# Performance work log

Measured on AMD Instinct MI355X. Metric: run time of the kernel, lower is better.

Reference implementation:

```python
import jax, jax.numpy as jnp
import numpy as np

LAYERS, BLOCKS = 10, 4
DC, RC, SC, CLASSES, K = 128, 128, 512, 256, 2
OUT_LEN = 2 ** (LAYERS - 1)  # 512
N, L = 4, 8192


def _dilations():
    # replicates the (new_dilation, init_dilation) schedule from __init__
    dils = []
    init_d = 1
    for _ in range(BLOCKS):
        d = 1
        for _ in range(LAYERS):
            dils.append((d, init_d))
            init_d = d
            d *= 2
    return dils


def conv1d(x, w):
    # x: (n, c_in, l), w: (c_out, c_in, k), VALID causal-style conv
    return jax.lax.conv_general_dilated(x, w, (1,), 'VALID',
                                        dimension_numbers=('NCH', 'OIH', 'NCH'))


def dilate(x, dilation, init_dilation):
    # fast-wavenet dilate: fold time phases into the batch dim (all shapes static)
    n, c, l = x.shape
    if dilation == init_dilation:
        return x
    if dilation > init_dilation:
        f = dilation // init_dilation
        new_l = -(-l // f) * f  # ceil to multiple of f
        if new_l != l:
            x = jnp.pad(x, ((0, 0), (0, 0), (new_l - l, 0)))  # zero-pad at start
            l = new_l
        l_new, n_new = l // f, n * f
    else:
        f = init_dilation // dilation
        l_new, n_new = l * f, n // f
    # (n,c,l) -> (c,l,n) -> (c,l_new,n_new) -> (n_new,c,l_new), matches torch view order
    x = jnp.transpose(x, (1, 2, 0)).reshape(c, l_new, n_new)
    return jnp.transpose(x, (2, 0, 1))


def setup_inputs() -> dict:
    key = jax.random.key(0)
    ks = jax.random.split(key, 7)
    NL = LAYERS * BLOCKS
    s = 0.05
    return {
        'input': jax.random.normal(ks[0], (N, 1, L), jnp.float32),
        'start_w': jax.random.normal(ks[1], (RC, 1, 1), jnp.float32) * s,
        'dilated_w': jax.random.normal(ks[2], (NL, 2 * DC, RC, K), jnp.float32) * s,
        'residual_w': jax.random.normal(ks[3], (NL, RC, DC, 1), jnp.float32) * s,
        'skip_w': jax.random.normal(ks[4], (NL, SC, DC, 1), jnp.float32) * s,
        'end_w': jax.random.normal(ks[5], (CLASSES, SC, 1), jnp.float32) * s,
        'end_b': jax.random.normal(ks[6], (CLASSES,), jnp.float32) * s,
    }


def reference(input, start_w, dilated_w, residual_w, skip_w, end_w, end_b):
    x = conv1d(input, start_w)
    skip = None
    for i, (d, init_d) in enumerate(_dilations()):
        residual = dilate(x, d, init_d)            # (n*d, RC, l_d)
        h = conv1d(residual, dilated_w[i])          # (n*d, 2*DC, l_d-1)
        h = jnp.tanh(h[:, :DC, :]) * jax.nn.sigmoid(h[:, DC:, :])
        s = dilate(h, 1, d) if h.shape[2] != 1 else h  # back to batch-major time
        s = conv1d(s, skip_w[i])
        skip = s if skip is None else s + skip[:, :, -s.shape[2]:]
        x = conv1d(h, residual_w[i]) + residual[:, :, K - 1:]
    out = conv1d(jax.nn.relu(skip), end_w) + end_b[None, :, None]
    n, c, _ = out.shape
    out = out[:, :, -OUT_LEN:]
    return jnp.transpose(out, (0, 2, 1)).reshape(n * OUT_LEN, c)
```

## Files before the change

### kernel.cpp

```cpp
#include <hip/hip_runtime.h>
#include <stdint.h>

#define NB 4
#define LSEQ 8192
#define TLOC 4608
#define TBASE 3584
#define NLAYER 40
#define SKIP_T0 4096
#define SKIP_LEN 512
#define NCLS 256

typedef float f32x4 __attribute__((ext_vector_type(4)));
typedef short bf16x8 __attribute__((ext_vector_type(8)));

typedef const __attribute__((address_space(1))) uint32_t GU32;
typedef __attribute__((address_space(3))) uint32_t LU32;

__device__ __forceinline__ void gload16(const void* g, void* l) {
    __builtin_amdgcn_global_load_lds((GU32*)g, (LU32*)l, 16, 0, 0);
}

__device__ __forceinline__ uint16_t f2bf(float x) {
    uint32_t u = __builtin_bit_cast(uint32_t, x);
    uint32_t r = (u + 0x7FFFu + ((u >> 16) & 1u)) >> 16;
    return (uint16_t)r;
}
__device__ __forceinline__ float bf2f(uint16_t h) {
    uint32_t u = ((uint32_t)h) << 16;
    return __builtin_bit_cast(float, u);
}
__device__ __forceinline__ uint2 pack4(const uint16_t a[4]) {
    return make_uint2((uint32_t)a[0] | ((uint32_t)a[1] << 16),
                      (uint32_t)a[2] | ((uint32_t)a[3] << 16));
}

__global__ __launch_bounds__(256) void k_prep_a(const float* __restrict__ Wd,
                                                uint16_t* __restrict__ AgH,
                                                uint16_t* __restrict__ AgL) {
    __shared__ float tile[32][257];
    int bi = blockIdx.x;
    int i = bi >> 3;
    int co0 = (bi & 7) * 32;
    int tid = threadIdx.x;
    #pragma unroll
    for (int e = 0; e < 32; ++e) {
        int idx = e * 256 + tid;
        int co_l = idx >> 8, rem = idx & 255;
        tile[co_l][rem] = Wd[(size_t)(i * 256 + co0 + co_l) * 256 + rem];
    }
    __syncthreads();
    #pragma unroll
    for (int e = 0; e < 32; ++e) {
        int co_l = e;
        int kk = tid;
        int ci = kk & 127, kt = kk >> 7;
        float v = tile[co_l][ci * 2 + kt];
        uint16_t h = f2bf(v);
        uint16_t lo = f2bf(v - bf2f(h));
        int co = co0 + co_l;
        int ch = kk >> 5, kkc = kk & 31;
        size_t o = ((size_t)(i * 8 + ch) * 256 + co) * 32 + (kkc ^ (((co >> 1) & 3) << 3));
        AgH[o] = h;
        AgL[o] = lo;
    }
}

__global__ __launch_bounds__(256) void k_prep_w(const float* __restrict__ Wr, const float* __restrict__ Ws,
                                                uint16_t* __restrict__ WrH, uint16_t* __restrict__ WrL,
                                                uint16_t* __restrict__ WsH, uint16_t* __restrict__ WsL) {
    int idx4 = (blockIdx.x * 256 + threadIdx.x) * 4;
    const int NR = NLAYER * 16384;
    const float* src = (idx4 < NR) ? (Wr + idx4) : (Ws + (idx4 - NR));
    uint16_t* dH = (idx4 < NR) ? (WrH + idx4) : (WsH + (idx4 - NR));
    uint16_t* dL = (idx4 < NR) ? (WrL + idx4) : (WsL + (idx4 - NR));
    float4 v = *(const float4*)src;
    uint16_t h[4], lo[4];
    float vv[4] = {v.x, v.y, v.z, v.w};
    #pragma unroll
    for (int r = 0; r < 4; ++r) {
        h[r] = f2bf(vv[r]);
        lo[r] = f2bf(vv[r] - bf2f(h[r]));
    }
    *(uint2*)dH = pack4(h);
    *(uint2*)dL = pack4(lo);
}

__global__ __launch_bounds__(256) void k_prep_e(const float* __restrict__ Ew,
                                                float* __restrict__ ET) {
    int idx = blockIdx.x * 256 + threadIdx.x;
    int cl = idx & 255;
    int sc = idx >> 8;
    ET[sc * 256 + cl] = Ew[cl * 512 + sc];
}

__global__ __launch_bounds__(256) void k_start(const float* __restrict__ input,
                                               const float* __restrict__ sw,
                                               uint16_t* __restrict__ Xh, uint16_t* __restrict__ Xl) {
    int n = blockIdx.y;
    int inner = blockIdx.x * 256 + threadIdx.x;
    int t = inner >> 7, c = inner & 127;
    float x = sw[c] * input[n * LSEQ + TBASE + t];
    uint16_t h = f2bf(x);
    size_t o = (size_t)(n * TLOC + t) * 128 + c;
    Xh[o] = h;
    Xl[o] = f2bf(x - bf2f(h));
}

__global__ __launch_bounds__(256, 2) void k_layer(
    const uint16_t* __restrict__ XhIn, const uint16_t* __restrict__ XlIn,
    uint16_t* __restrict__ XhOut, uint16_t* __restrict__ XlOut,
    float* __restrict__ skipbuf,
    const uint16_t* __restrict__ AgH, const uint16_t* __restrict__ AgL,
    const uint16_t* __restrict__ WrH, const uint16_t* __restrict__ WrL,
    const uint16_t* __restrict__ WsH, const uint16_t* __restrict__ WsL,
    int d)
{
    __shared__ uint16_t As[2][16384];
    __shared__ uint16_t Bs[2][2048];

    const int tid = threadIdx.x;
    const int w  = tid >> 6;
    const int l  = tid & 63;
    const int g  = l >> 4;
    const int lq = l & 15;
    const int tb = 143 - blockIdx.x;
    const int t0 = tb * 32;
    const int nb = blockIdx.y;

    f32x4 acc[2][2][2];
    #pragma unroll
    for (int pm = 0; pm < 2; ++pm)
        #pragma unroll
        for (int mi = 0; mi < 2; ++mi)
            #pragma unroll
            for (int ni = 0; ni < 2; ++ni)
                acc[pm][mi][ni] = (f32x4){0.f, 0.f, 0.f, 0.f};

#define STAGE(ch, buf) do {                                                             \
    _Pragma("unroll")                                                                   \
    for (int j = 0; j < 4; ++j) {                                                       \
        gload16(AgH + (size_t)(ch) * 8192 + (j * 256 + tid) * 8,                        \
                &As[buf][(j * 256 + tid) * 8]);                                         \
        gload16(AgL + (size_t)(ch) * 8192 + (j * 256 + tid) * 8,                        \
                &As[buf][8192 + (j * 256 + tid) * 8]);                                  \
    }                                                                                   \
    {   int s = tid & 127;                                                              \
        int b = s * 16;                                                                 \
        int tt = b >> 6;                                                                \
        int e = (b & 63) ^ (((tt >> 1) & 3) << 4);                                      \
        int ci = (((ch) & 3) << 5) + (e >> 1);                                          \
        int t = t0 + tt - (((ch) < 4) ? d : 0);                                         \
        if (t < 0) t = 0;                                                               \
        size_t gi = (size_t)(nb * TLOC + t) * 128 + ci;                                 \
        if (tid < 128) gload16(XhIn + gi, &Bs[buf][s * 8]);                             \
        else           gload16(XlIn + gi, &Bs[buf][1024 + s * 8]);                      \
    } } while (0)

    STAGE(0, 0);
    #pragma unroll
    for (int ch = 0; ch < 8; ++ch) {
        __syncthreads();
        if (ch < 7) STAGE(ch + 1, (ch + 1) & 1);
        const uint16_t* AsH = &As[ch & 1][0];
        const uint16_t* AsL = &As[ch & 1][8192];
        const uint16_t* BsH = &Bs[ch & 1][0];
        const uint16_t* BsL = &Bs[ch & 1][1024];

        bf16x8 Bh[2], Bl[2];
        #pragma unroll
        for (int ni = 0; ni < 2; ++ni) {
            int tt = ni * 16 + lq;
            int byte = (tt * 64 + g * 16) ^ (((tt >> 1) & 3) << 4);
            Bh[ni] = *(const bf16x8*)((const char*)BsH + byte);
            Bl[ni] = *(const bf16x8*)((const char*)BsL + byte);
        }
        bf16x8 Ah[2][2], Al[2][2];
        #pragma unroll
        for (int pm = 0; pm < 2; ++pm)
            #pragma unroll
            for (int mi = 0; mi < 2; ++mi) {
                int co = pm * 128 + w * 32 + mi * 16 + lq;
                int byte = (co * 64 + g * 16) ^ (((co >> 1) & 3) << 4);
                Ah[pm][mi] = *(const bf16x8*)((const char*)AsH + byte);
                Al[pm][mi] = *(const bf16x8*)((const char*)AsL + byte);
            }
        #pragma unroll
        for (int pm = 0; pm < 2; ++pm)
            #pragma unroll
            for (int mi = 0; mi < 2; ++mi)
                #pragma unroll
                for (int ni = 0; ni < 2; ++ni) {
                    f32x4 c = acc[pm][mi][ni];
                    c = __builtin_amdgcn_mfma_f32_16x16x32_bf16(Ah[pm][mi], Bh[ni], c, 0, 0, 0);
                    c = __builtin_amdgcn_mfma_f32_16x16x32_bf16(Ah[pm][mi], Bl[ni], c, 0, 0, 0);
                    c = __builtin_amdgcn_mfma_f32_16x16x32_bf16(Al[pm][mi], Bh[ni], c, 0, 0, 0);
                    acc[pm][mi][ni] = c;
                }
    }
#undef STAGE

    bf16x8 wrh[2][4], wrl[2][4];
    #pragma unroll
    for (int mi = 0; mi < 2; ++mi) {
        int rc = w * 32 + mi * 16 + lq;
        #pragma unroll
        for (int c4 = 0; c4 < 4; ++c4) {
            int dc0 = c4 * 32 + g * 8;
            wrh[mi][c4] = *(const bf16x8*)(WrH + rc * 128 + dc0);
            wrl[mi][c4] = *(const bf16x8*)(WrL + rc * 128 + dc0);
        }
    }

    uint16_t* ZtH = &As[0][0];
    uint16_t* ZtL = &As[0][4096];
    #pragma unroll
    for (int mi = 0; mi < 2; ++mi)
        #pragma unroll
        for (int ni = 0; ni < 2; ++ni) {
            uint16_t zh[4], zl[4];
            #pragma unroll
            for (int r = 0; r < 4; ++r) {
                float h1 = acc[0][mi][ni][r];
                float h2 = acc[1][mi][ni][r];
                float e1 = __builtin_amdgcn_exp2f(h1 * -2.885390082f);
                float th = 2.0f * __builtin_amdgcn_rcpf(1.0f + e1) - 1.0f;
                float e2 = __builtin_amdgcn_exp2f(h2 * -1.442695041f);
                float sg = __builtin_amdgcn_rcpf(1.0f + e2);
                float z = th * sg;
                zh[r] = f2bf(z);
                zl[r] = f2bf(z - bf2f(zh[r]));
            }
            int tt = ni * 16 + lq;
            int dc0 = w * 32 + mi * 16 + g * 4;
            int idx = tt * 128 + (dc0 ^ ((tt & 7) << 3));
            *(uint2*)(ZtH + idx) = pack4(zh);
            *(uint2*)(ZtL + idx) = pack4(zl);
        }
    __syncthreads();

    f32x4 racc[2][2];
    #pragma unroll
    for (int mi = 0; mi < 2; ++mi)
        #pragma unroll
        for (int ni = 0; ni < 2; ++ni)
            racc[mi][ni] = (f32x4){0.f, 0.f, 0.f, 0.f};
    #pragma unroll
    for (int c4 = 0; c4 < 4; ++c4) {
        int dc0 = c4 * 32 + g * 8;
        bf16x8 bh[2], bl[2];
        #pragma unroll
        for (int ni = 0; ni < 2; ++ni) {
            int tt = ni * 16 + lq;
            int idx = tt * 128 + (dc0 ^ ((tt & 7) << 3));
            bh[ni] = *(const bf16x8*)(ZtH + idx);
            bl[ni] = *(const bf16x8*)(ZtL + idx);
        }
        #pragma unroll
        for (int mi = 0; mi < 2; ++mi)
            #pragma unroll
            for (int ni = 0; ni < 2; ++ni) {
                f32x4 c = racc[mi][ni];
                c = __builtin_amdgcn_mfma_f32_16x16x32_bf16(wrh[mi][c4], bh[ni], c, 0, 0, 0);
                c = __builtin_amdgcn_mfma_f32_16x16x32_bf16(wrh[mi][c4], bl[ni], c, 0, 0, 0);
                c = __builtin_amdgcn_mfma_f32_16x16x32_bf16(wrl[mi][c4], bh[ni], c, 0, 0, 0);
                racc[mi][ni] = c;
            }
    }
    #pragma unroll
    for (int mi = 0; mi < 2; ++mi)
        #pragma unroll
        for (int ni = 0; ni < 2; ++ni) {
            int tt = ni * 16 + lq;
            int c0 = w * 32 + mi * 16 + g * 4;
            size_t gi = (size_t)(nb * TLOC + t0 + tt) * 128 + c0;
            uint2 xh = *(const uint2*)(XhIn + gi);
            uint2 xl = *(const uint2*)(XlIn + gi);
            uint16_t oh[4], ol[4];
            #pragma unroll
            for (int r = 0; r < 4; ++r) {
                uint16_t hh = (uint16_t)(((r < 2 ? xh.x : xh.y) >> ((r & 1) * 16)) & 0xFFFF);
                uint16_t ll = (uint16_t)(((r < 2 ? xl.x : xl.y) >> ((r & 1) * 16)) & 0xFFFF);
                float x = bf2f(hh) + bf2f(ll) + racc[mi][ni][r];
                oh[r] = f2bf(x);
                ol[r] = f2bf(x - bf2f(oh[r]));
            }
            *(uint2*)(XhOut + gi) = pack4(oh);
            *(uint2*)(XlOut + gi) = pack4(ol);
        }

    if (t0 >= SKIP_T0) {
        #pragma unroll
        for (int hf = 0; hf < 2; ++hf) {
            f32x4 sacc[4][2];
            #pragma unroll
            for (int mi = 0; mi < 4; ++mi)
                #pragma unroll
                for (int ni = 0; ni < 2; ++ni)
                    sacc[mi][ni] = (f32x4){0.f, 0.f, 0.f, 0.f};
            #pragma unroll
            for (int c4 = 0; c4 < 4; ++c4) {
                int dc0 = c4 * 32 + g * 8;
                bf16x8 bh[2], bl[2];
                #pragma unroll
                for (int ni = 0; ni < 2; ++ni) {
                    int tt = ni * 16 + lq;
                    int idx = tt * 128 + (dc0 ^ ((tt & 7) << 3));
                    bh[ni] = *(const bf16x8*)(ZtH + idx);
                    bl[ni] = *(const bf16x8*)(ZtL + idx);
                }
                #pragma unroll
                for (int mi = 0; mi < 4; ++mi) {
                    int sc = hf * 256 + w * 64 + mi * 16 + lq;
                    bf16x8 ah = *(const bf16x8*)(WsH + sc * 128 + dc0);
                    bf16x8 al = *(const bf16x8*)(WsL + sc * 128 + dc0);
                    #pragma unroll
                    for (int ni = 0; ni < 2; ++ni) {
                        f32x4 c = sacc[mi][ni];
                        c = __builtin_amdgcn_mfma_f32_16x16x32_bf16(ah, bh[ni], c, 0, 0, 0);
                        c = __builtin_amdgcn_mfma_f32_16x16x32_bf16(ah, bl[ni], c, 0, 0, 0);
                        c = __builtin_amdgcn_mfma_f32_16x16x32_bf16(al, bh[ni], c, 0, 0, 0);
                        sacc[mi][ni] = c;
                    }
                }
            }
            #pragma unroll
            for (int mi = 0; mi < 4; ++mi)
                #pragma unroll
                for (int ni = 0; ni < 2; ++ni)
                    #pragma unroll
                    for (int r = 0; r < 4; ++r) {
                        int sc = hf * 256 + w * 64 + mi * 16 + g * 4 + r;
                        int ts = t0 - SKIP_T0 + ni * 16 + lq;
                        skipbuf[sc * (NB * SKIP_LEN) + nb * SKIP_LEN + ts] += sacc[mi][ni][r];
                    }
        }
    }
}

__global__ __launch_bounds__(256) void k_end1(const float* __restrict__ skipbuf,
                                              const float* __restrict__ ET,
                                              float* __restrict__ partial) {
    __shared__ float ss[128][17];
    int bx = blockIdx.x;
    int scq = bx >> 7;
    int n = (bx >> 5) & 3;
    int tt0 = (bx & 31) * 16;
    int tid = threadIdx.x;
    #pragma unroll
    for (int e = 0; e < 8; ++e) {
        int idx = e * 256 + tid;
        int sc_l = idx >> 4, tt = idx & 15;
        float v = skipbuf[(scq * 128 + sc_l) * (NB * SKIP_LEN) + n * SKIP_LEN + tt0 + tt];
        ss[sc_l][tt] = fmaxf(v, 0.f);
    }
    __syncthreads();
    float accv[16];
    #pragma unroll
    for (int i = 0; i < 16; ++i) accv[i] = 0.f;
    #pragma unroll 4
    for (int sc_l = 0; sc_l < 128; ++sc_l) {
        float wv = ET[(scq * 128 + sc_l) * 256 + tid];
        #pragma unroll
        for (int i = 0; i < 16; ++i) accv[i] = fmaf(wv, ss[sc_l][i], accv[i]);
    }
    #pragma unroll
    for (int i = 0; i < 16; ++i)
        partial[((size_t)scq * 2048 + n * 512 + tt0 + i) * 256 + tid] = accv[i];
}

__global__ __launch_bounds__(256) void k_end2(const float* __restrict__ partial,
                                              const float* __restrict__ Eb,
                                              float* __restrict__ out) {
    int o = blockIdx.x * 256 + threadIdx.x;
    float v = Eb[threadIdx.x];
    #pragma unroll
    for (int q = 0; q < 4; ++q) v += partial[(size_t)q * 524288 + o];
    out[o] = v;
}

extern "C" void kernel_launch(void* const* d_in, const int* in_sizes, int n_in,
                              void* d_out, int out_size, void* d_ws, size_t ws_size,
                              hipStream_t stream) {
    const float* input      = (const float*)d_in[0];
    const float* start_w    = (const float*)d_in[1];
    const float* dilated_w  = (const float*)d_in[2];
    const float* residual_w = (const float*)d_in[3];
    const float* skip_w     = (const float*)d_in[4];
    const float* end_w      = (const float*)d_in[5];
    const float* end_b      = (const float*)d_in[6];
    float* out = (float*)d_out;

    uint8_t* w8 = (uint8_t*)d_ws;
    uint16_t* Xh0   = (uint16_t*)(w8);
    uint16_t* Xl0   = (uint16_t*)(w8 + 4718592);
    uint16_t* Xh1   = (uint16_t*)(w8 + 9437184);
    uint16_t* Xl1   = (uint16_t*)(w8 + 14155776);
    float*    skipb = (float*)   (w8 + 18874368);
    uint16_t* AgH   = (uint16_t*)(w8 + 23068672);
    uint16_t* AgL   = (uint16_t*)(w8 + 28311552);
    uint16_t* WrH   = (uint16_t*)(w8 + 33554432);
    uint16_t* WrL   = (uint16_t*)(w8 + 34865152);
    uint16_t* WsH   = (uint16_t*)(w8 + 36175872);
    uint16_t* WsL   = (uint16_t*)(w8 + 41418752);
    float*    ET    = (float*)   (w8 + 46661632);
    float*    partial = (float*)w8;

    hipMemsetAsync(skipb, 0, (size_t)512 * NB * SKIP_LEN * sizeof(float), stream);
    k_prep_a<<<dim3(320), 256, 0, stream>>>(dilated_w, AgH, AgL);
    k_prep_w<<<dim3(3200), 256, 0, stream>>>(residual_w, skip_w, WrH, WrL, WsH, WsL);
    k_prep_e<<<dim3(512), 256, 0, stream>>>(end_w, ET);
    k_start<<<dim3(2304, 4), 256, 0, stream>>>(input, start_w, Xh0, Xl0);

    for (int i = 0; i < NLAYER; ++i) {
        int d = 1 << (i % 10);
        const uint16_t* ih = (i & 1) ? Xh1 : Xh0;
        const uint16_t* il = (i & 1) ? Xl1 : Xl0;
        uint16_t* oh = (i & 1) ? Xh0 : Xh1;
        uint16_t* ol = (i & 1) ? Xl0 : Xl1;
        k_layer<<<dim3(144, 4), 256, 0, stream>>>(
            ih, il, oh, ol, skipb,
            AgH + (size_t)i * 65536, AgL + (size_t)i * 65536,
            WrH + (size_t)i * 16384, WrL + (size_t)i * 16384,
            WsH + (size_t)i * 65536, WsL + (size_t)i * 65536,
            d);
    }
    k_end1<<<dim3(512), 256, 0, stream>>>(skipb, ET, partial);
    k_end2<<<dim3(2048), 256, 0, stream>>>(partial, end_b, out);
}
```

Measured before the change: 1.302 ms.

## Process two batch items per layer block to reuse staged weights

Each layer block now covers 32 time steps for two batch items (64 columns) rather than one, and the grid is halved in y. The staged dilated-conv weight tiles and the residual/skip weights are therefore loaded once per two batch items, cutting global-to-LDS weight traffic per output. The cost is a grid of 288 blocks instead of 576, which may underfill the GPU's compute units, plus larger accumulator arrays that raise register pressure under launch_bounds(256,2).

```diff
diff --git a/kernel.cpp b/kernel.cpp
--- a/kernel.cpp
+++ b/kernel.cpp
@@ -116,7 +116,7 @@
     int d)
 {
     __shared__ uint16_t As[2][16384];
-    __shared__ uint16_t Bs[2][2048];
+    __shared__ uint16_t Bs[2][4096];
 
     const int tid = threadIdx.x;
     const int w  = tid >> 6;
@@ -125,15 +125,15 @@
     const int lq = l & 15;
     const int tb = 143 - blockIdx.x;
     const int t0 = tb * 32;
-    const int nb = blockIdx.y;
-
-    f32x4 acc[2][2][2];
+    const int nb2 = blockIdx.y;
+
+    f32x4 acc[2][2][4];
     #pragma unroll
     for (int pm = 0; pm < 2; ++pm)
         #pragma unroll
         for (int mi = 0; mi < 2; ++mi)
             #pragma unroll
-            for (int ni = 0; ni < 2; ++ni)
+            for (int ni = 0; ni < 4; ++ni)
                 acc[pm][mi][ni] = (f32x4){0.f, 0.f, 0.f, 0.f};
 
 #define STAGE(ch, buf) do {                                                             \
@@ -144,16 +144,16 @@
         gload16(AgL + (size_t)(ch) * 8192 + (j * 256 + tid) * 8,                        \
                 &As[buf][8192 + (j * 256 + tid) * 8]);                                  \
     }                                                                                   \
-    {   int s = tid & 127;                                                              \
-        int b = s * 16;                                                                 \
-        int tt = b >> 6;                                                                \
-        int e = (b & 63) ^ (((tt >> 1) & 3) << 4);                                      \
+    {   int b = tid * 16;                                      \
+        int col = b >> 6;                                           \
+        int e = (b & 63) ^ (((col >> 1) & 3) << 4);                                     \
         int ci = (((ch) & 3) << 5) + (e >> 1);                                          \
+        int m = col >> 5, tt = col & 31;                                                \
         int t = t0 + tt - (((ch) < 4) ? d : 0);                                         \
         if (t < 0) t = 0;                                                               \
-        size_t gi = (size_t)(nb * TLOC + t) * 128 + ci;                                 \
-        if (tid < 128) gload16(XhIn + gi, &Bs[buf][s * 8]);                             \
-        else           gload16(XlIn + gi, &Bs[buf][1024 + s * 8]);                      \
+        size_t gi = (size_t)((nb2 * 2 + m) * TLOC + t) * 128 + ci;                      \
+        gload16(XhIn + gi, &Bs[buf][tid * 8]);                                          \
+        gload16(XlIn + gi, &Bs[buf][2048 + tid * 8]);                                   \
     } } while (0)
 
     STAGE(0, 0);
@@ -164,13 +164,13 @@
         const uint16_t* AsH = &As[ch & 1][0];
         const uint16_t* AsL = &As[ch & 1][8192];
         const uint16_t* BsH = &Bs[ch & 1][0];
-        const uint16_t* BsL = &Bs[ch & 1][1024];
-
-        bf16x8 Bh[2], Bl[2];
-        #pragma unroll
-        for (int ni = 0; ni < 2; ++ni) {
-            int tt = ni * 16 + lq;
-            int byte = (tt * 64 + g * 16) ^ (((tt >> 1) & 3) << 4);
+        const uint16_t* BsL = &Bs[ch & 1][2048];
+
+        bf16x8 Bh[4], Bl[4];
+        #pragma unroll
+        for (int ni = 0; ni < 4; ++ni) {
+            int col = ni * 16 + lq;
+            int byte = (col * 64 + g * 16) ^ (((col >> 1) & 3) << 4);
             Bh[ni] = *(const bf16x8*)((const char*)BsH + byte);
             Bl[ni] = *(const bf16x8*)((const char*)BsL + byte);
         }
@@ -189,7 +189,7 @@
             #pragma unroll
             for (int mi = 0; mi < 2; ++mi)
                 #pragma unroll
-                for (int ni = 0; ni < 2; ++ni) {
+                for (int ni = 0; ni < 4; ++ni) {
                     f32x4 c = acc[pm][mi][ni];
                     c = __builtin_amdgcn_mfma_f32_16x16x32_bf16(Ah[pm][mi], Bh[ni], c, 0, 0, 0);
                     c = __builtin_amdgcn_mfma_f32_16x16x32_bf16(Ah[pm][mi], Bl[ni], c, 0, 0, 0);
@@ -212,11 +212,11 @@
     }
 
     uint16_t* ZtH = &As[0][0];
-    uint16_t* ZtL = &As[0][4096];
+    uint16_t* ZtL = &As[0][8192];
     #pragma unroll
     for (int mi = 0; mi < 2; ++mi)
         #pragma unroll
-        for (int ni = 0; ni < 2; ++ni) {
+        for (int ni = 0; ni < 4; ++ni) {
             uint16_t zh[4], zl[4];
             #pragma unroll
             for (int r = 0; r < 4; ++r) {
@@ -230,35 +230,35 @@
                 zh[r] = f2bf(z);
                 zl[r] = f2bf(z - bf2f(zh[r]));
             }
-            int tt = ni * 16 + lq;
+            int col = ni * 16 + lq;
             int dc0 = w * 32 + mi * 16 + g * 4;
-            int idx = tt * 128 + (dc0 ^ ((tt & 7) << 3));
+            int idx = col * 128 + (dc0 ^ ((col & 7) << 3));
             *(uint2*)(ZtH + idx) = pack4(zh);
             *(uint2*)(ZtL + idx) = pack4(zl);
         }
     __syncthreads();
 
-    f32x4 racc[2][2];
+    f32x4 racc[2][4];
     #pragma unroll
     for (int mi = 0; mi < 2; ++mi)
         #pragma unroll
-        for (int ni = 0; ni < 2; ++ni)
+        for (int ni = 0; ni < 4; ++ni)
             racc[mi][ni] = (f32x4){0.f, 0.f, 0.f, 0.f};
     #pragma unroll
     for (int c4 = 0; c4 < 4; ++c4) {
         int dc0 = c4 * 32 + g * 8;
-        bf16x8 bh[2], bl[2];
-        #pragma unroll
-        for (int ni = 0; ni < 2; ++ni) {
-            int tt = ni * 16 + lq;
-            int idx = tt * 128 + (dc0 ^ ((tt & 7) << 3));
+        bf16x8 bh[4], bl[4];
+        #pragma unroll
+        for (int ni = 0; ni < 4; ++ni) {
+            int col = ni * 16 + lq;
+            int idx = col * 128 + (dc0 ^ ((col & 7) << 3));
             bh[ni] = *(const bf16x8*)(ZtH + idx);
             bl[ni] = *(const bf16x8*)(ZtL + idx);
         }
         #pragma unroll
         for (int mi = 0; mi < 2; ++mi)
             #pragma unroll
-            for (int ni = 0; ni < 2; ++ni) {
+            for (int ni = 0; ni < 4; ++ni) {
                 f32x4 c = racc[mi][ni];
                 c = __builtin_amdgcn_mfma_f32_16x16x32_bf16(wrh[mi][c4], bh[ni], c, 0, 0, 0);
                 c = __builtin_amdgcn_mfma_f32_16x16x32_bf16(wrh[mi][c4], bl[ni], c, 0, 0, 0);
@@ -269,10 +269,12 @@
     #pragma unroll
     for (int mi = 0; mi < 2; ++mi)
         #pragma unroll
-        for (int ni = 0; ni < 2; ++ni) {
-            int tt = ni * 16 + lq;
+        for (int ni = 0; ni < 4; ++ni) {
+            int col = ni * 16 + lq;
+            int n = nb2 * 2 + (col >> 5);
+            int t = t0 + (col & 31);
             int c0 = w * 32 + mi * 16 + g * 4;
-            size_t gi = (size_t)(nb * TLOC + t0 + tt) * 128 + c0;
+            size_t gi = (size_t)(n * TLOC + t) * 128 + c0;
             uint2 xh = *(const uint2*)(XhIn + gi);
             uint2 xl = *(const uint2*)(XlIn + gi);
             uint16_t oh[4], ol[4];
@@ -291,20 +293,20 @@
     if (t0 >= SKIP_T0) {
         #pragma unroll
         for (int hf = 0; hf < 2; ++hf) {
-            f32x4 sacc[4][2];
+            f32x4 sacc[4][4];
             #pragma unroll
             for (int mi = 0; mi < 4; ++mi)
                 #pragma unroll
-                for (int ni = 0; ni < 2; ++ni)
+                for (int ni = 0; ni < 4; ++ni)
                     sacc[mi][ni] = (f32x4){0.f, 0.f, 0.f, 0.f};
             #pragma unroll
             for (int c4 = 0; c4 < 4; ++c4) {
                 int dc0 = c4 * 32 + g * 8;
-                bf16x8 bh[2], bl[2];
+                bf16x8 bh[4], bl[4];
                 #pragma unroll
-                for (int ni = 0; ni < 2; ++ni) {
-                    int tt = ni * 16 + lq;
-                    int idx = tt * 128 + (dc0 ^ ((tt & 7) << 3));
+                for (int ni = 0; ni < 4; ++ni) {
+                    int col = ni * 16 + lq;
+                    int idx = col * 128 + (dc0 ^ ((col & 7) << 3));
                     bh[ni] = *(const bf16x8*)(ZtH + idx);
                     bl[ni] = *(const bf16x8*)(ZtL + idx);
                 }
@@ -314,7 +316,7 @@
                     bf16x8 ah = *(const bf16x8*)(WsH + sc * 128 + dc0);
                     bf16x8 al = *(const bf16x8*)(WsL + sc * 128 + dc0);
                     #pragma unroll
-                    for (int ni = 0; ni < 2; ++ni) {
+                    for (int ni = 0; ni < 4; ++ni) {
                         f32x4 c = sacc[mi][ni];
                         c = __builtin_amdgcn_mfma_f32_16x16x32_bf16(ah, bh[ni], c, 0, 0, 0);
                         c = __builtin_amdgcn_mfma_f32_16x16x32_bf16(ah, bl[ni], c, 0, 0, 0);
@@ -326,12 +328,14 @@
             #pragma unroll
             for (int mi = 0; mi < 4; ++mi)
                 #pragma unroll
-                for (int ni = 0; ni < 2; ++ni)
+                for (int ni = 0; ni < 4; ++ni)
                     #pragma unroll
                     for (int r = 0; r < 4; ++r) {
                         int sc = hf * 256 + w * 64 + mi * 16 + g * 4 + r;
-                        int ts = t0 - SKIP_T0 + ni * 16 + lq;
-                        skipbuf[sc * (NB * SKIP_LEN) + nb * SKIP_LEN + ts] += sacc[mi][ni][r];
+                        int col = ni * 16 + lq;
+                        int n = nb2 * 2 + (col >> 5);
+                        int ts = t0 - SKIP_T0 + (col & 31);
+                        skipbuf[sc * (NB * SKIP_LEN) + n * SKIP_LEN + ts] += sacc[mi][ni][r];
                     }
         }
     }
@@ -417,7 +421,7 @@
         const uint16_t* il = (i & 1) ? Xl1 : Xl0;
         uint16_t* oh = (i & 1) ? Xh0 : Xh1;
         uint16_t* ol = (i & 1) ? Xl0 : Xl1;
-        k_layer<<<dim3(144, 4), 256, 0, stream>>>(
+        k_layer<<<dim3(144, 2), 256, 0, stream>>>(
             ih, il, oh, ol, skipb,
             AgH + (size_t)i * 65536, AgL + (size_t)i * 65536,
             WrH + (size_t)i * 16384, WrL + (size_t)i * 16384,
```

After: 1.354 ms. +4.0%, slower.
